# Performance work log

Measured on AMD Instinct MI355X. Metric: run time of the kernel, lower is better.

Reference implementation:

```python
import jax, jax.numpy as jnp
import numpy as np

B, S, H, NH = 2, 2048, 1024, 16
HD = H // NH
BASE = 10000.0


def _rotate_half(x):
    x1, x2 = x[..., : x.shape[-1] // 2], x[..., x.shape[-1] // 2 :]
    return jnp.concatenate((-x2, x1), axis=-1)


def setup_inputs() -> dict:
    key = jax.random.key(0)
    ks = jax.random.split(key, 6)
    hidden_states = jax.random.normal(ks[0], (B, S, H), jnp.float32)
    scale = 0.02
    wq = jax.random.normal(ks[1], (H, H), jnp.float32) * scale
    wk = jax.random.normal(ks[2], (H, H), jnp.float32) * scale
    wv = jax.random.normal(ks[3], (H, H), jnp.float32) * scale
    wo = jax.random.normal(ks[4], (H, H), jnp.float32) * scale
    # additive causal mask, shape (B, 1, S, S): 0 on/below diagonal, large negative above
    neg = jnp.finfo(jnp.float32).min
    causal = jnp.where(jnp.tril(jnp.ones((S, S), dtype=bool)), 0.0, neg).astype(jnp.float32)
    attention_mask = jnp.broadcast_to(causal[None, None], (B, 1, S, S))
    position_ids = jnp.broadcast_to(jnp.arange(S, dtype=jnp.int32)[None], (B, S))
    return {
        "hidden_states": hidden_states,
        "attention_mask": attention_mask,
        "wq": wq,
        "wk": wk,
        "wv": wv,
        "wo": wo,
        "position_ids": position_ids,
    }


def reference(hidden_states, attention_mask, wq, wk, wv, wo, position_ids):
    b, s, h = hidden_states.shape
    dtype = hidden_states.dtype

    def proj(x, w):  # torch Linear: y = x @ w.T, then split heads -> (b, nh, s, hd)
        y = jnp.einsum("bsh,oh->bso", x, w)
        return y.reshape(b, s, NH, HD).transpose(0, 2, 1, 3)

    q = proj(hidden_states, wq)
    k = proj(hidden_states, wk)
    v = proj(hidden_states, wv)

    # rotary cache (computed in fp32 like torch), gathered by position_ids
    inv_freq = 1.0 / (BASE ** (jnp.arange(0, HD, 2, dtype=jnp.float32) / HD))
    t = jnp.arange(s, dtype=jnp.float32)
    freqs = jnp.outer(t, inv_freq)                  # (s, hd/2)
    emb = jnp.concatenate((freqs, freqs), axis=-1)  # (s, hd)
    pos = jnp.clip(position_ids, 0, s - 1)
    cos = jnp.cos(emb).astype(dtype)[pos][:, None]  # (b, 1, s, hd)
    sin = jnp.sin(emb).astype(dtype)[pos][:, None]

    q = q * cos + _rotate_half(q) * sin
    k = k * cos + _rotate_half(k) * sin

    scores = jnp.einsum("bhqd,bhkd->bhqk", q, k) / jnp.sqrt(jnp.asarray(HD, dtype))
    scores = scores + attention_mask
    attn = jax.nn.softmax(scores.astype(jnp.float32), axis=-1).astype(dtype)
    out = jnp.einsum("bhqk,bhkd->bhqd", attn, v)    # (b, nh, s, hd)
    out = out.transpose(0, 2, 1, 3).reshape(b, s, h)
    return jnp.einsum("bso,ho->bsh", out, wo)
```

## Files before the change

kernel.cpp:

```cpp
#include <hip/hip_runtime.h>
#include <cstdint>
#include <cstddef>

typedef unsigned short u16;
typedef __bf16 bf16x8 __attribute__((ext_vector_type(8)));
typedef float f32x4 __attribute__((ext_vector_type(4)));

constexpr int SEQ = 2048;
constexpr int HID = 1024;
constexpr int NHEAD = 16;
constexpr int HDIM = 64;

typedef __attribute__((address_space(1))) void gvoid;
typedef __attribute__((address_space(3))) void lvoid;

__device__ __forceinline__ u16 f2bf(float f) {
  union { float f; unsigned u; } v;
  v.f = f;
  unsigned r = v.u + 0x7fffu + ((v.u >> 16) & 1u);
  return (u16)(r >> 16);
}
__device__ __forceinline__ u16 f2bf_trunc(float f) {
  union { float f; unsigned u; } v;
  v.f = f;
  return (u16)(v.u >> 16);
}

__device__ __forceinline__ f32x4 mfma16(bf16x8 a, bf16x8 b, f32x4 c) {
  return __builtin_amdgcn_mfma_f32_16x16x32_bf16(a, b, c, 0, 0, 0);
}

__device__ __forceinline__ int detect_f32(const unsigned* __restrict__ hs) {
  unsigned w = hs[threadIdx.x & 63];
  u16 lo = (u16)(w & 0xffffu);
  int e = (lo >> 7) & 0xff;
  bool inr = (e >= 100 && e <= 154);
  unsigned long long m = __ballot(inr);
  return (__popcll(m) >= 48) ? 0 : 1;
}

__global__ __launch_bounds__(256) void cvt_kernel(
    const void* s0, const void* s1, const void* s2, const void* s3, const void* s4,
    u16* __restrict__ d0, u16* __restrict__ dW,
    float* __restrict__ cosb, float* __restrict__ sinb) {
  int b = blockIdx.x;
  if (b >= 4096) {
    int idx = (b - 4096) * 256 + threadIdx.x;
    int s = idx >> 5;
    int i = idx & 31;
    float inv_freq = expf(-(float)(2 * i) * (9.210340371976184f / 64.0f));
    float ang = (float)s * inv_freq;
    float c = cosf(ang), sn = sinf(ang);
    cosb[s * 64 + i]      = c;
    cosb[s * 64 + i + 32] = c;
    sinb[s * 64 + i]      = sn;
    sinb[s * 64 + i + 32] = sn;
    return;
  }
  const int is_f32 = detect_f32((const unsigned*)s0);
  const void* s; u16* d; long base;
  if (b < 2048) { s = s0; d = d0; base = (long)b * 2048; }
  else {
    int bb = b - 2048;
    int w = bb >> 9;
    base = (long)(bb & 511) * 2048;
    s = (w == 0) ? s1 : (w == 1) ? s2 : (w == 2) ? s3 : s4;
    d = dW + (long)w * 1048576;
  }
  long idx = base + (long)threadIdx.x * 8;
  if (is_f32) {
    const float* sf = (const float*)s;
    float4 a = *(const float4*)(sf + idx);
    float4 c = *(const float4*)(sf + idx + 4);
    ushort4 p0, p1;
    p0.x = f2bf(a.x); p0.y = f2bf(a.y); p0.z = f2bf(a.z); p0.w = f2bf(a.w);
    p1.x = f2bf(c.x); p1.y = f2bf(c.y); p1.z = f2bf(c.z); p1.w = f2bf(c.w);
    *(ushort4*)(d + idx) = p0;
    *(ushort4*)(d + idx + 4) = p1;
  } else {
    const u16* su = (const u16*)s;
    *(uint4*)(d + idx) = *(const uint4*)(su + idx);
  }
}

__device__ __forceinline__ void gemm_mainloop_256(
    const u16* __restrict__ Ag, const u16* __restrict__ Bg,
    int row0, int col0, f32x4 acc[8][4]) {
  __shared__ __align__(16) u16 As[2][256 * 64];
  __shared__ __align__(16) u16 Bs[2][256 * 64];
  const int t = threadIdx.x;
  const int lane = t & 63, wave = t >> 6;
  const int l15 = lane & 15, quad = lane >> 4;
  const int wm = wave >> 2, wn = wave & 3;
  const int srow = lane >> 3;
  const int cs = ((lane & 7) ^ srow) * 8;
  const u16* aS = Ag + (size_t)(row0 + wave * 32 + srow) * 1024 + cs;
  const u16* bS = Bg + (size_t)(col0 + wave * 32 + srow) * 1024 + cs;
  const int swz0 = ((quad)     ^ (l15 & 7)) * 8;
  const int swz1 = ((4 + quad) ^ (l15 & 7)) * 8;

#define STAGE_A(bi, k0_) do {                                                    \
    _Pragma("unroll")                                                            \
    for (int j = 0; j < 4; j++)                                                  \
      __builtin_amdgcn_global_load_lds((gvoid*)(aS + (k0_) + j * 8192),          \
          (lvoid*)(&As[bi][0] + wave * 2048 + j * 512), 16, 0, 0);               \
  } while (0)
#define STAGE_B(bi, k0_) do {                                                    \
    _Pragma("unroll")                                                            \
    for (int j = 0; j < 4; j++)                                                  \
      __builtin_amdgcn_global_load_lds((gvoid*)(bS + (k0_) + j * 8192),          \
          (lvoid*)(&Bs[bi][0] + wave * 2048 + j * 512), 16, 0, 0);               \
  } while (0)
#define PBAR() do {                                                              \
    __builtin_amdgcn_sched_barrier(0);                                           \
    __builtin_amdgcn_s_barrier();                                                \
    __builtin_amdgcn_sched_barrier(0);                                           \
  } while (0)
#define READ_AF(QM) do {                                                         \
    _Pragma("unroll")                                                            \
    for (int mi = 0; mi < 4; mi++) {                                             \
      const u16* ap = Ab + (wm * 128 + (QM) * 64 + mi * 16 + l15) * 64;          \
      af[mi][0] = *(const bf16x8*)(ap + swz0);                                   \
      af[mi][1] = *(const bf16x8*)(ap + swz1);                                   \
    }                                                                            \
  } while (0)
#define READ_BF(NB) do {                                                         \
    _Pragma("unroll")                                                            \
    for (int nj = 0; nj < 2; nj++) {                                             \
      const u16* bp = Bb + (wn * 64 + ((NB) + nj) * 16 + l15) * 64;              \
      bfr[nj][0] = *(const bf16x8*)(bp + swz0);                                  \
      bfr[nj][1] = *(const bf16x8*)(bp + swz1);                                  \
    }                                                                            \
  } while (0)
#define MFMA_PH(QM, NB) do {                                                     \
    __builtin_amdgcn_s_setprio(1);                                               \
    _Pragma("unroll")                                                            \
    for (int mi = 0; mi < 4; mi++)                                               \
    _Pragma("unroll")                                                            \
    for (int nj = 0; nj < 2; nj++)                                               \
    _Pragma("unroll")                                                            \
    for (int kk = 0; kk < 2; kk++)                                               \
      acc[(QM) * 4 + mi][(NB) + nj] =                                            \
          mfma16(af[mi][kk], bfr[nj][kk], acc[(QM) * 4 + mi][(NB) + nj]);        \
    __builtin_amdgcn_s_setprio(0);                                               \
  } while (0)

  STAGE_A(0, 0);
  STAGE_B(0, 0);
  asm volatile("s_waitcnt vmcnt(0)" ::: "memory");
  PBAR();

  for (int kt = 0; kt < 16; ++kt) {
    const int cur = kt & 1;
    const u16* Ab = &As[cur][0];
    const u16* Bb = &Bs[cur][0];
    const bool pf = (kt + 1 < 16);
    bf16x8 af[4][2], bfr[2][2];
    READ_AF(0); READ_BF(0);
    if (pf) STAGE_A(cur ^ 1, (kt + 1) * 64);
    PBAR();
    MFMA_PH(0, 0);
    PBAR();
    READ_BF(2);
    if (pf) STAGE_B(cur ^ 1, (kt + 1) * 64);
    PBAR();
    MFMA_PH(0, 2);
    PBAR();
    READ_AF(1); READ_BF(0);
    PBAR();
    MFMA_PH(1, 0);
    PBAR();
    READ_BF(2);
    PBAR();
    MFMA_PH(1, 2);
    if (pf) asm volatile("s_waitcnt vmcnt(0)" ::: "memory");
    PBAR();
  }
#undef STAGE_A
#undef STAGE_B
#undef PBAR
#undef READ_AF
#undef READ_BF
#undef MFMA_PH
}

__global__ __launch_bounds__(512, 2) void qkv_kernel(
    const u16* __restrict__ X, const u16* __restrict__ Wcat,
    const int* __restrict__ pos_ids,
    const float* __restrict__ cosb, const float* __restrict__ sinb,
    u16* __restrict__ q_ws, u16* __restrict__ k_ws, u16* __restrict__ vt_ws) {
  const int row0 = blockIdx.x * 256;
  const int col0 = blockIdx.y * 256;
  f32x4 acc[8][4];
#pragma unroll
  for (int i = 0; i < 8; i++)
#pragma unroll
    for (int j = 0; j < 4; j++) acc[i][j] = f32x4{0.f, 0.f, 0.f, 0.f};

  gemm_mainloop_256(X, Wcat, row0, col0, acc);

  const int t = threadIdx.x;
  const int lane = t & 63, wave = t >> 6;
  const int l15 = lane & 15, quad = lane >> 4;
  const int wm = wave >> 2, wn = wave & 3;
  const int gr0 = row0 + wm * 128;
  const int gc0 = col0 + wn * 64;
  const int z = gc0 >> 10;
  const int nh = (gc0 >> 6) & 15;
  const float qscale = (z == 0) ? 0.18033688011112042f : 1.0f;

  if (z < 2) {
    u16* dst = (z == 0) ? q_ws : k_ws;
#pragma unroll
    for (int i = 0; i < 8; i++) {
#pragma unroll
      for (int r = 0; r < 4; r++) {
        int m = gr0 + i * 16 + quad * 4 + r;
        int b = m >> 11, s = m & 2047;
        int p = pos_ids[m];
        p = min(max(p, 0), SEQ - 1);
#pragma unroll
        for (int j = 0; j < 4; j++) {
          int d = j * 16 + l15;
          float c = cosb[p * 64 + d];
          float sn = sinb[p * 64 + d];
          float v = acc[i][j][r];
          float partner = acc[i][j ^ 2][r];
          float rot = (j < 2) ? -partner : partner;
          float o = (v * c + rot * sn) * qscale;
          dst[((size_t)((b * NHEAD + nh) * SEQ + s) << 6) + d] = f2bf(o);
        }
      }
    }
  } else {
#pragma unroll
    for (int i = 0; i < 8; i++) {
      int m_base = gr0 + i * 16 + quad * 4;
      int b = m_base >> 11, s = m_base & 2047;
#pragma unroll
      for (int j = 0; j < 4; j++) {
        int d = j * 16 + l15;
        ushort4 pk;
        pk.x = f2bf(acc[i][j][0]);
        pk.y = f2bf(acc[i][j][1]);
        pk.z = f2bf(acc[i][j][2]);
        pk.w = f2bf(acc[i][j][3]);
        *(ushort4*)(vt_ws + ((size_t)((b * NHEAD + nh) * 64 + d)) * SEQ + s) = pk;
      }
    }
  }
}

__global__ __launch_bounds__(256) void attn_kernel(
    const u16* __restrict__ q_ws, const u16* __restrict__ k_ws,
    const u16* __restrict__ vt_ws, u16* __restrict__ attn_ws) {
  const int b = blockIdx.z;
  const int qt = b ? blockIdx.x : 15 - blockIdx.x;
  const int nh = blockIdx.y;
  const int bh = b * NHEAD + nh;
  __shared__ __align__(16) u16 Ks[2][128 * 64];
  __shared__ __align__(16) u16 Vts[2][64 * 128];
  __shared__ __align__(16) u16 Pl[128 * 64];

  const int t = threadIdx.x;
  const int lane = t & 63, wave = t >> 6;
  const int l15 = lane & 15, quad = lane >> 4;
  const int l7 = l15 & 7;
  const int wq0 = qt * 128 + wave * 32;

  bf16x8 aq[2][2];
#pragma unroll
  for (int i = 0; i < 2; i++) {
    const u16* qb = q_ws + ((size_t)bh * SEQ + wq0 + i * 16 + l15) * 64;
    aq[i][0] = *(const bf16x8*)(qb + quad * 8);
    aq[i][1] = *(const bf16x8*)(qb + 32 + quad * 8);
  }

  f32x4 O[2][4];
  float lp[2];
#pragma unroll
  for (int i = 0; i < 2; i++) {
    lp[i] = 0.f;
#pragma unroll
    for (int n = 0; n < 4; n++) O[i][n] = f32x4{0.f, 0.f, 0.f, 0.f};
  }

  const int krl = lane >> 3;
  const int kcs = ((lane & 7) ^ (krl & 7)) * 8;
  const u16* kS = k_ws + (size_t)bh * SEQ * 64 + (size_t)(wave * 32 + krl) * 64 + kcs;
  const int vrl = lane >> 4;
  const int vc4 = lane & 15;
  const u16* vS = vt_ws + (size_t)bh * 64 * SEQ + (size_t)(wave * 16 + vrl) * SEQ;
  int vx[4];
#pragma unroll
  for (int j = 0; j < 4; j++) vx[j] = (vc4 ^ ((4 * j + vrl) & 15)) * 8;

#define STAGE_KV(bi, kt_) do {                                                     \
    const size_t koff_ = (size_t)(kt_) * 8192;                                     \
    _Pragma("unroll")                                                              \
    for (int j = 0; j < 4; j++) {                                                  \
      __builtin_amdgcn_global_load_lds((gvoid*)(kS + koff_ + j * 512),             \
          (lvoid*)(&Ks[bi][0] + wave * 2048 + j * 512), 16, 0, 0);                 \
      __builtin_amdgcn_global_load_lds(                                            \
          (gvoid*)(vS + (size_t)j * 4 * SEQ + (kt_) * 128 + vx[j]),                \
          (lvoid*)(&Vts[bi][0] + wave * 2048 + j * 512), 16, 0, 0);                \
    }                                                                              \
  } while (0)

  const int nkt = qt + 1;
  STAGE_KV(0, 0);
  int cur = 0;
  for (int kt = 0; kt < nkt; ++kt) {
    if (kt + 1 < nkt) {
      STAGE_KV(cur ^ 1, kt + 1);
      asm volatile("s_waitcnt vmcnt(8)" ::: "memory");
    } else {
      asm volatile("s_waitcnt vmcnt(0)" ::: "memory");
    }
    __builtin_amdgcn_sched_barrier(0);
    __builtin_amdgcn_s_barrier();
    __builtin_amdgcn_sched_barrier(0);
    const u16* Ksb = &Ks[cur][0];
    const u16* Vtb = &Vts[cur][0];

#pragma unroll
    for (int h = 0; h < 2; h++) {
      f32x4 sc[2][4];
      __builtin_amdgcn_s_setprio(1);
#pragma unroll
      for (int ct = 0; ct < 4; ct++) {
        const u16* krow = Ksb + (h * 64 + ct * 16 + l15) * 64;
        bf16x8 bk0 = *(const bf16x8*)(krow + (quad ^ l7) * 8);
        bf16x8 bk1 = *(const bf16x8*)(krow + ((4 + quad) ^ l7) * 8);
#pragma unroll
        for (int i = 0; i < 2; i++) {
          f32x4 z = f32x4{0.f, 0.f, 0.f, 0.f};
          z = mfma16(bk0, aq[i][0], z);
          z = mfma16(bk1, aq[i][1], z);
          sc[i][ct] = z;
        }
      }
      __builtin_amdgcn_s_setprio(0);

      const int kbase = kt * 128 + h * 64;
      if (kt == qt) {
#pragma unroll
        for (int i = 0; i < 2; i++) {
          const int qrow = wq0 + i * 16 + l15;
          const int prow = (wave * 32 + i * 16 + l15) * 64;
#pragma unroll
          for (int ct = 0; ct < 4; ct++) {
            const int key0 = kbase + ct * 16 + quad * 4;
            float p[4];
#pragma unroll
            for (int r = 0; r < 4; r++) {
              float e = __builtin_amdgcn_exp2f(sc[i][ct][r]);
              if (key0 + r > qrow) e = 0.f;
              p[r] = e;
            }
            lp[i] += (p[0] + p[1]) + (p[2] + p[3]);
            ushort4 pk;
            pk.x = f2bf_trunc(p[0]); pk.y = f2bf_trunc(p[1]);
            pk.z = f2bf_trunc(p[2]); pk.w = f2bf_trunc(p[3]);
            *(ushort4*)&Pl[prow + ((ct * 2 + (quad >> 1)) ^ l7) * 8 + (quad & 1) * 4] = pk;
          }
        }
      } else {
#pragma unroll
        for (int i = 0; i < 2; i++) {
          const int prow = (wave * 32 + i * 16 + l15) * 64;
#pragma unroll
          for (int ct = 0; ct < 4; ct++) {
            float p[4];
#pragma unroll
            for (int r = 0; r < 4; r++) p[r] = __builtin_amdgcn_exp2f(sc[i][ct][r]);
            lp[i] += (p[0] + p[1]) + (p[2] + p[3]);
            ushort4 pk;
            pk.x = f2bf_trunc(p[0]); pk.y = f2bf_trunc(p[1]);
            pk.z = f2bf_trunc(p[2]); pk.w = f2bf_trunc(p[3]);
            *(ushort4*)&Pl[prow + ((ct * 2 + (quad >> 1)) ^ l7) * 8 + (quad & 1) * 4] = pk;
          }
        }
      }

      bf16x8 pa[2][2];
#pragma unroll
      for (int i = 0; i < 2; i++) {
        const u16* prow = Pl + (wave * 32 + i * 16 + l15) * 64;
        pa[i][0] = *(const bf16x8*)(prow + (quad ^ l7) * 8);
        pa[i][1] = *(const bf16x8*)(prow + ((4 + quad) ^ l7) * 8);
      }
      __builtin_amdgcn_s_setprio(1);
#pragma unroll
      for (int n = 0; n < 4; n++) {
        const u16* vrow = Vtb + (n * 16 + l15) * 128;
        bf16x8 bv0 = *(const bf16x8*)(vrow + ((h * 8 + quad) ^ l15) * 8);
        bf16x8 bv1 = *(const bf16x8*)(vrow + ((h * 8 + 4 + quad) ^ l15) * 8);
#pragma unroll
        for (int i = 0; i < 2; i++) {
          O[i][n] = mfma16(pa[i][0], bv0, O[i][n]);
          O[i][n] = mfma16(pa[i][1], bv1, O[i][n]);
        }
      }
      __builtin_amdgcn_s_setprio(0);
    }

    __builtin_amdgcn_sched_barrier(0);
    __builtin_amdgcn_s_barrier();
    __builtin_amdgcn_sched_barrier(0);
    cur ^= 1;
  }
#undef STAGE_KV

#pragma unroll
  for (int i = 0; i < 2; i++) {
    float l = lp[i];
    l += __shfl_xor(l, 16, 64);
    l += __shfl_xor(l, 32, 64);
#pragma unroll
    for (int r = 0; r < 4; r++) {
      float inv = 1.0f / __shfl(l, quad * 4 + r, 64);
      int q = wq0 + i * 16 + quad * 4 + r;
      size_t base = ((size_t)(b * SEQ + q)) * HID + nh * 64;
#pragma unroll
      for (int n = 0; n < 4; n++)
        attn_ws[base + n * 16 + l15] = f2bf(O[i][n][r] * inv);
    }
  }
}

__global__ __launch_bounds__(256) void out_proj_kernel(
    const u16* __restrict__ A, const u16* __restrict__ Wo, void* __restrict__ out,
    const unsigned* __restrict__ hs_raw) {
  __shared__ __align__(16) u16 As[2][128 * 64];
  __shared__ __align__(16) u16 Bs[2][128 * 64];
  const int row0 = blockIdx.x * 128;
  const int col0 = blockIdx.y * 128;
  const int is_f32 = detect_f32(hs_raw);
  const int t = threadIdx.x;
  const int lane = t & 63, wave = t >> 6;
  const int l15 = lane & 15, quad = lane >> 4;
  const int wm = wave >> 1, wn = wave & 1;
  const int cs = ((lane & 7) ^ ((lane >> 3) & 7)) * 8;
  const u16* aS = A  + (size_t)(row0 + wave * 32 + (lane >> 3)) * 1024 + cs;
  const u16* bS = Wo + (size_t)(col0 + wave * 32 + (lane >> 3)) * 1024 + cs;
  const int swz0 = ((quad)     ^ (l15 & 7)) * 8;
  const int swz1 = ((4 + quad) ^ (l15 & 7)) * 8;

  f32x4 acc[4][4];
#pragma unroll
  for (int i = 0; i < 4; i++)
#pragma unroll
    for (int j = 0; j < 4; j++) acc[i][j] = f32x4{0.f, 0.f, 0.f, 0.f};

#define STAGE_AB(bi, k0_) do {                                                   \
    _Pragma("unroll")                                                            \
    for (int j = 0; j < 4; j++) {                                                \
      __builtin_amdgcn_global_load_lds((gvoid*)(aS + (k0_) + j * 8192),          \
          (lvoid*)(&As[bi][0] + wave * 2048 + j * 512), 16, 0, 0);               \
      __builtin_amdgcn_global_load_lds((gvoid*)(bS + (k0_) + j * 8192),          \
          (lvoid*)(&Bs[bi][0] + wave * 2048 + j * 512), 16, 0, 0);               \
    }                                                                            \
  } while (0)

  STAGE_AB(0, 0);
  int cur = 0;
  for (int k0 = 0; k0 < 1024; k0 += 64) {
    if (k0 + 64 < 1024) {
      STAGE_AB(cur ^ 1, k0 + 64);
      asm volatile("s_waitcnt vmcnt(8)" ::: "memory");
    } else {
      asm volatile("s_waitcnt vmcnt(0)" ::: "memory");
    }
    __builtin_amdgcn_sched_barrier(0);
    __builtin_amdgcn_s_barrier();
    __builtin_amdgcn_sched_barrier(0);
    const u16* Asb = &As[cur][0];
    const u16* Bsb = &Bs[cur][0];
#pragma unroll
    for (int kk = 0; kk < 2; kk++) {
      const int sw = kk ? swz1 : swz0;
      bf16x8 af[4], bfr[4];
#pragma unroll
      for (int i = 0; i < 4; i++)
        af[i] = *(const bf16x8*)(Asb + (wm * 64 + i * 16 + l15) * 64 + sw);
#pragma unroll
      for (int j = 0; j < 4; j++)
        bfr[j] = *(const bf16x8*)(Bsb + (wn * 64 + j * 16 + l15) * 64 + sw);
#pragma unroll
      for (int i = 0; i < 4; i++)
#pragma unroll
        for (int j = 0; j < 4; j++)
          acc[i][j] = mfma16(af[i], bfr[j], acc[i][j]);
    }
    __builtin_amdgcn_sched_barrier(0);
    __builtin_amdgcn_s_barrier();
    __builtin_amdgcn_sched_barrier(0);
    cur ^= 1;
  }
#undef STAGE_AB

  const int gr0 = row0 + wm * 64;
  const int gc0 = col0 + wn * 64;
#pragma unroll
  for (int i = 0; i < 4; i++)
#pragma unroll
    for (int r = 0; r < 4; r++) {
      int m = gr0 + i * 16 + quad * 4 + r;
      if (is_f32) {
        float* o = (float*)out;
#pragma unroll
        for (int j = 0; j < 4; j++)
          o[(size_t)m * 1024 + gc0 + j * 16 + l15] = acc[i][j][r];
      } else {
        u16* o = (u16*)out;
#pragma unroll
        for (int j = 0; j < 4; j++)
          o[(size_t)m * 1024 + gc0 + j * 16 + l15] = f2bf(acc[i][j][r]);
      }
    }
}

extern "C" void kernel_launch(void* const* d_in, const int* in_sizes, int n_in,
                              void* d_out, int out_size, void* d_ws, size_t ws_size,
                              hipStream_t stream) {
  const void* hs = d_in[0];
  const void* wq = d_in[2];
  const void* wk = d_in[3];
  const void* wv = d_in[4];
  const void* wo = d_in[5];
  const int* pos = (const int*)d_in[6];

  char* ws = (char*)d_ws;
  float* cosb = (float*)ws;
  float* sinb = (float*)(ws + (512 << 10));
  u16* xbf    = (u16*)(ws + (1 << 20));
  u16* wcat   = xbf + (size_t)4194304;
  u16* q_ws   = wcat + (size_t)4 * 1048576;
  u16* k_ws   = q_ws + (size_t)2 * NHEAD * SEQ * HDIM;
  u16* vt_ws  = k_ws + (size_t)2 * NHEAD * SEQ * HDIM;
  u16* attn_ws = vt_ws + (size_t)2 * NHEAD * SEQ * HDIM;

  cvt_kernel<<<4352, 256, 0, stream>>>(hs, wq, wk, wv, wo, xbf, wcat, cosb, sinb);
  qkv_kernel<<<dim3(16, 12), 512, 0, stream>>>(xbf, wcat, pos, cosb, sinb,
                                               q_ws, k_ws, vt_ws);
  attn_kernel<<<dim3(16, NHEAD, 2), 256, 0, stream>>>(q_ws, k_ws, vt_ws, attn_ws);
  out_proj_kernel<<<dim3(32, 8), 256, 0, stream>>>(attn_ws, wcat + (size_t)3 * 1048576,
                                                   d_out, (const unsigned*)hs);
}
```

Baseline: 202.2 us.

## Shrink QKV GEMM tile to 256x192 with six waves to fill all CUs

```diff
diff --git a/kernel.cpp b/kernel.cpp
--- a/kernel.cpp
+++ b/kernel.cpp
@@ -83,33 +83,49 @@
   }
 }
 
-__device__ __forceinline__ void gemm_mainloop_256(
+__device__ __forceinline__ void gemm_mainloop_256x192(
     const u16* __restrict__ Ag, const u16* __restrict__ Bg,
     int row0, int col0, f32x4 acc[8][4]) {
   __shared__ __align__(16) u16 As[2][256 * 64];
-  __shared__ __align__(16) u16 Bs[2][256 * 64];
+  __shared__ __align__(16) u16 Bs[2][192 * 64];
   const int t = threadIdx.x;
   const int lane = t & 63, wave = t >> 6;
   const int l15 = lane & 15, quad = lane >> 4;
-  const int wm = wave >> 2, wn = wave & 3;
+  const int wm = wave / 3, wn = wave % 3;
   const int srow = lane >> 3;
   const int cs = ((lane & 7) ^ srow) * 8;
-  const u16* aS = Ag + (size_t)(row0 + wave * 32 + srow) * 1024 + cs;
-  const u16* bS = Bg + (size_t)(col0 + wave * 32 + srow) * 1024 + cs;
+  const bool isA = (wave < 4);
+  const int wb = wave - 4;
+  const u16* aS = Ag + (size_t)(row0 + wave * 64 + srow) * 1024 + cs;
+  const u16* bS = Bg + (size_t)(col0 + wb * 96 + srow) * 1024 + cs;
   const int swz0 = ((quad)     ^ (l15 & 7)) * 8;
   const int swz1 = ((4 + quad) ^ (l15 & 7)) * 8;
 
-#define STAGE_A(bi, k0_) do {                                                    \
-    _Pragma("unroll")                                                            \
-    for (int j = 0; j < 4; j++)                                                  \
-      __builtin_amdgcn_global_load_lds((gvoid*)(aS + (k0_) + j * 8192),          \
-          (lvoid*)(&As[bi][0] + wave * 2048 + j * 512), 16, 0, 0);               \
-  } while (0)
-#define STAGE_B(bi, k0_) do {                                                    \
-    _Pragma("unroll")                                                            \
-    for (int j = 0; j < 4; j++)                                                  \
-      __builtin_amdgcn_global_load_lds((gvoid*)(bS + (k0_) + j * 8192),          \
-          (lvoid*)(&Bs[bi][0] + wave * 2048 + j * 512), 16, 0, 0);               \
+#define STAGE_P0(bi, k0_) do {                                                   \
+    if (isA) {                                                                   \
+      _Pragma("unroll")                                                          \
+      for (int j = 0; j < 4; j++)                                                \
+        __builtin_amdgcn_global_load_lds((gvoid*)(aS + (k0_) + j * 8192),        \
+            (lvoid*)(&As[bi][0] + wave * 4096 + j * 512), 16, 0, 0);             \
+    } else {                                                                     \
+      _Pragma("unroll")                                                          \
+      for (int j = 0; j < 6; j++)                                                \
+        __builtin_amdgcn_global_load_lds((gvoid*)(bS + (k0_) + j * 8192),        \
+            (lvoid*)(&Bs[bi][0] + wb * 6144 + j * 512), 16, 0, 0);               \
+    }                                                                            \
+  } while (0)
+#define STAGE_P1(bi, k0_) do {                                                   \
+    if (isA) {                                                                   \
+      _Pragma("unroll")                                                          \
+      for (int j = 4; j < 8; j++)                                                \
+        __builtin_amdgcn_global_load_lds((gvoid*)(aS + (k0_) + j * 8192),        \
+            (lvoid*)(&As[bi][0] + wave * 4096 + j * 512), 16, 0, 0);             \
+    } else {                                                                     \
+      _Pragma("unroll")                                                          \
+      for (int j = 6; j < 12; j++)                                               \
+        __builtin_amdgcn_global_load_lds((gvoid*)(bS + (k0_) + j * 8192),        \
+            (lvoid*)(&Bs[bi][0] + wb * 6144 + j * 512), 16, 0, 0);               \
+    }                                                                            \
   } while (0)
 #define PBAR() do {                                                              \
     __builtin_amdgcn_sched_barrier(0);                                           \
@@ -145,8 +161,8 @@
     __builtin_amdgcn_s_setprio(0);                                               \
   } while (0)
 
-  STAGE_A(0, 0);
-  STAGE_B(0, 0);
+  STAGE_P0(0, 0);
+  STAGE_P1(0, 0);
   asm volatile("s_waitcnt vmcnt(0)" ::: "memory");
   PBAR();
 
@@ -157,12 +173,12 @@
     const bool pf = (kt + 1 < 16);
     bf16x8 af[4][2], bfr[2][2];
     READ_AF(0); READ_BF(0);
-    if (pf) STAGE_A(cur ^ 1, (kt + 1) * 64);
+    if (pf) STAGE_P0(cur ^ 1, (kt + 1) * 64);
     PBAR();
     MFMA_PH(0, 0);
     PBAR();
     READ_BF(2);
-    if (pf) STAGE_B(cur ^ 1, (kt + 1) * 64);
+    if (pf) STAGE_P1(cur ^ 1, (kt + 1) * 64);
     PBAR();
     MFMA_PH(0, 2);
     PBAR();
@@ -176,33 +192,33 @@
     if (pf) asm volatile("s_waitcnt vmcnt(0)" ::: "memory");
     PBAR();
   }
-#undef STAGE_A
-#undef STAGE_B
+#undef STAGE_P0
+#undef STAGE_P1
 #undef PBAR
 #undef READ_AF
 #undef READ_BF
 #undef MFMA_PH
 }
 
-__global__ __launch_bounds__(512, 2) void qkv_kernel(
+__global__ __launch_bounds__(384) void qkv_kernel(
     const u16* __restrict__ X, const u16* __restrict__ Wcat,
     const int* __restrict__ pos_ids,
     const float* __restrict__ cosb, const float* __restrict__ sinb,
     u16* __restrict__ q_ws, u16* __restrict__ k_ws, u16* __restrict__ vt_ws) {
   const int row0 = blockIdx.x * 256;
-  const int col0 = blockIdx.y * 256;
+  const int col0 = blockIdx.y * 192;
   f32x4 acc[8][4];
 #pragma unroll
   for (int i = 0; i < 8; i++)
 #pragma unroll
     for (int j = 0; j < 4; j++) acc[i][j] = f32x4{0.f, 0.f, 0.f, 0.f};
 
-  gemm_mainloop_256(X, Wcat, row0, col0, acc);
+  gemm_mainloop_256x192(X, Wcat, row0, col0, acc);
 
   const int t = threadIdx.x;
   const int lane = t & 63, wave = t >> 6;
   const int l15 = lane & 15, quad = lane >> 4;
-  const int wm = wave >> 2, wn = wave & 3;
+  const int wm = wave / 3, wn = wave % 3;
   const int gr0 = row0 + wm * 128;
   const int gc0 = col0 + wn * 64;
   const int z = gc0 >> 10;
@@ -542,7 +558,7 @@
   u16* attn_ws = vt_ws + (size_t)2 * NHEAD * SEQ * HDIM;
 
   cvt_kernel<<<4352, 256, 0, stream>>>(hs, wq, wk, wv, wo, xbf, wcat, cosb, sinb);
-  qkv_kernel<<<dim3(16, 12), 512, 0, stream>>>(xbf, wcat, pos, cosb, sinb,
+  qkv_kernel<<<dim3(16, 16), 384, 0, stream>>>(xbf, wcat, pos, cosb, sinb,
                                                q_ws, k_ws, vt_ws);
   attn_kernel<<<dim3(16, NHEAD, 2), 256, 0, stream>>>(q_ws, k_ws, vt_ws, attn_ws);
   out_proj_kernel<<<dim3(32, 8), 256, 0, stream>>>(attn_ws, wcat + (size_t)3 * 1048576,
```

Measured after the change: 197.9 us. 2.1% less time.
